# Optimization experiments

Hardware: AMD Instinct MI355X
Metric: run time of the kernel (lower is better)

The kernel has to match this reference:

```python
import jax, jax.numpy as jnp
import numpy as np

B, C, H, E, K, QT = 256, 1024, 64, 64, 2, 20000

def _mlp(x, W1, b1, W2, b2):
    # GKT MLP (eval mode: dropout off; batch-norm omitted, see notes)
    return jax.nn.relu(jax.nn.relu(x @ W1 + b1) @ W2 + b2)

def setup_inputs() -> dict:
    key = jax.random.key(0)
    ks = jax.random.split(key, 30)
    s = 0.05  # weight scale to keep pre-clamp activations in a sane range
    xt = jax.random.uniform(ks[0], (B,), dtype=jnp.float32)
    qt = jax.random.randint(ks[1], (B,), 0, QT)
    ht = jax.random.normal(ks[2], (B, C, H), dtype=jnp.float32)
    # binary question->concept incidence, ~4 KCs per question, col 0 forced on
    oh = (jax.random.uniform(ks[3], (QT, C)) < 4.0 / C).astype(jnp.float32)
    oh = oh.at[:, 0].set(1.0)
    qt_kc_one_hot = jnp.concatenate([oh, jnp.zeros((1, C), jnp.float32)], axis=0)  # zero padding row
    kc_embeddings = jax.random.normal(ks[4], (C, E), dtype=jnp.float32) * 0.1
    graphs = jax.random.uniform(ks[5], (K, C, C), dtype=jnp.float32)  # graph_model output
    neigh_weight = jnp.float32(0.8)
    MI = H + E
    Ws1 = jax.random.normal(ks[6], (MI, H), jnp.float32) * s; bs1 = jnp.zeros((H,), jnp.float32)
    Ws2 = jax.random.normal(ks[7], (H, H), jnp.float32) * s;  bs2 = jnp.zeros((H,), jnp.float32)
    Wn1 = jax.random.normal(ks[8], (K, 2 * MI, H), jnp.float32) * s; bn1 = jnp.zeros((K, H), jnp.float32)
    Wn2 = jax.random.normal(ks[9], (K, H, H), jnp.float32) * s;      bn2 = jnp.zeros((K, H), jnp.float32)
    ea_w = jax.random.uniform(ks[10], (C,), dtype=jnp.float32)
    We = jax.random.normal(ks[11], (H, H), jnp.float32) * s; be = jnp.zeros((H,), jnp.float32)
    Wa = jax.random.normal(ks[12], (H, H), jnp.float32) * s; ba = jnp.zeros((H,), jnp.float32)
    W_ih = jax.random.normal(ks[13], (H, 3 * H), jnp.float32) * s; b_ih = jnp.zeros((3 * H,), jnp.float32)
    W_hh = jax.random.normal(ks[14], (H, 3 * H), jnp.float32) * s; b_hh = jnp.zeros((3 * H,), jnp.float32)
    Wp = jax.random.normal(ks[15], (H, 1), jnp.float32) * s; bp = jnp.zeros((1,), jnp.float32)
    return dict(xt=xt, qt=qt, ht=ht, qt_kc_one_hot=qt_kc_one_hot, kc_embeddings=kc_embeddings,
                graphs=graphs, neigh_weight=neigh_weight, Ws1=Ws1, bs1=bs1, Ws2=Ws2, bs2=bs2,
                Wn1=Wn1, bn1=bn1, Wn2=Wn2, bn2=bn2, ea_w=ea_w, We=We, be=be, Wa=Wa, ba=ba,
                W_ih=W_ih, b_ih=b_ih, W_hh=W_hh, b_hh=b_hh, Wp=Wp, bp=bp)

def reference(xt, qt, ht, qt_kc_one_hot, kc_embeddings, graphs, neigh_weight,
              Ws1, bs1, Ws2, bs2, Wn1, bn1, Wn2, bn2, ea_w, We, be, Wa, ba,
              W_ih, b_ih, W_hh, b_hh, Wp, bp):
    # ---- _aggregate: the fusion loops never write back, so tmp_ht = cat(ht, kc_emb)
    mask = qt_kc_one_hot[qt]                                   # [B, C] gather of binary incidence
    kc = jnp.broadcast_to(kc_embeddings[None], (mask.shape[0], C, E))
    tmp_ht = jnp.concatenate([ht, kc], axis=-1)                # [B, C, H+E]
    # ---- _agg_neighbors
    self_ht = tmp_ht * mask[..., None]
    self_feat = jnp.clip(_mlp(self_ht, Ws1, bs1, Ws2, bs2), -10.0, 10.0)
    neigh_ht = jnp.clip(jnp.concatenate([self_ht, tmp_ht], axis=-1), -5.0, 5.0)  # [B,C,2(H+E)]
    # bug-faithful adj: mean of graphs[k] rows over sample 0's active concepts
    a0 = mask[0]                                               # [C]
    denom = jnp.maximum(a0.sum(), 1.0)
    adj = jnp.clip(jnp.einsum('c,kcd->kd', a0, graphs) / denom, -5.0, 5.0)       # [K, C]
    nb = jax.vmap(lambda W1, b1, W2, b2: _mlp(neigh_ht, W1, b1, W2, b2))(Wn1, bn1, Wn2, bn2)
    nb = jnp.clip(nb, -5.0, 5.0)                               # [K, B, C, H]
    w = jnp.clip(neigh_weight, 0.1, 0.9)
    nf = jnp.clip(adj[0][None, :, None] * nb[0], -5.0, 5.0)
    for k in range(1, K):
        nf = jnp.clip(w * nf + (1.0 - w) * adj[k][None, :, None] * nb[k], -5.0, 5.0)
    m_next = jnp.clip(jnp.where(mask[..., None] > 0.5, self_feat, nf), -50.0, 50.0)
    # ---- erase-add gate
    g = ea_w[None, :, None]
    res = m_next - g * jax.nn.sigmoid(m_next @ We + be) * m_next + g * jnp.tanh(m_next @ Wa + ba)
    # ---- GRUCell over flattened (B*C) rows
    gi = res @ W_ih + b_ih
    gh = ht @ W_hh + b_hh
    ir, iz, in_ = jnp.split(gi, 3, axis=-1)
    hr, hz, hn = jnp.split(gh, 3, axis=-1)
    r = jax.nn.sigmoid(ir + hr)
    z = jax.nn.sigmoid(iz + hz)
    n = jnp.tanh(in_ + r * hn)
    h_next = (1.0 - z) * n + z * ht                            # [B, C, H]
    y = jax.nn.sigmoid(h_next @ Wp + bp)[..., 0]               # [B, C]
    return y
```

## Files before the change

### kernel.cpp

```cpp
#include <hip/hip_runtime.h>

#define DEVINL __device__ __forceinline__

typedef __bf16 bf16x8 __attribute__((ext_vector_type(8)));
typedef float  f32x4  __attribute__((ext_vector_type(4)));
typedef unsigned u32x2 __attribute__((ext_vector_type(2)));

static constexpr size_t kAdjOff  = 0;
static constexpr size_t kBiasOff = 8192;
static constexpr size_t kFragOff = 8192 + 786432;

static constexpr int FB_Wn1h0 = 0,  FB_Wn1h1 = 8,  FB_Wn2_0 = 16, FB_Wn2_1 = 24;
static constexpr int FB_Ws1h  = 32, FB_Ws2   = 40, FB_We    = 48, FB_Wa    = 56;
static constexpr int FB_Wih   = 64, FB_Whh   = 88;

DEVINL unsigned short bf16r(float f) {
  unsigned u = __builtin_bit_cast(unsigned, f);
  unsigned r = ((u >> 16) & 1u) + 0x7FFFu;
  return (unsigned short)((u + r) >> 16);
}
DEVINL float sigmoidf_(float x) { return __builtin_amdgcn_rcpf(1.f + __expf(-x)); }
DEVINL float tanhf_(float x)    { return 1.f - 2.f * __builtin_amdgcn_rcpf(1.f + __expf(2.f * x)); }

DEVINL unsigned pkbf(float a, float b) {
  unsigned d;
  asm("v_cvt_pk_bf16_f32 %0, %1, %2" : "=v"(d) : "v"(a), "v"(b));
  return d;
}

DEVINL f32x4 mfma16(bf16x8 a, bf16x8 b, f32x4 c) {
  return __builtin_amdgcn_mfma_f32_16x16x32_bf16(a, b, c, 0, 0, 0);
}

DEVINL unsigned clip2_(unsigned x) {
  float lo = __builtin_bit_cast(float, x << 16);
  float hi = __builtin_bit_cast(float, x & 0xFFFF0000u);
  lo = fminf(fmaxf(lo, -5.f), 5.f);
  hi = fminf(fmaxf(hi, -5.f), 5.f);
  return (__builtin_bit_cast(unsigned, lo) >> 16) | (__builtin_bit_cast(unsigned, hi) & 0xFFFF0000u);
}
DEVINL bf16x8 clip5(bf16x8 a) {
  uint4 u = __builtin_bit_cast(uint4, a);
  u.x = clip2_(u.x); u.y = clip2_(u.y); u.z = clip2_(u.z); u.w = clip2_(u.w);
  return __builtin_bit_cast(bf16x8, u);
}

DEVINL void ldA2_tr(unsigned addr, bf16x8& a0, bf16x8& a1) {
  u32x2 r0, r1, r2, r3;
  asm volatile(
      "ds_read_b64_tr_b16 %0, %4\n\t"
      "ds_read_b64_tr_b16 %1, %4 offset:512\n\t"
      "ds_read_b64_tr_b16 %2, %4 offset:1024\n\t"
      "ds_read_b64_tr_b16 %3, %4 offset:1536\n\t"
      "s_waitcnt lgkmcnt(0)"
      : "=&v"(r0), "=&v"(r1), "=&v"(r2), "=&v"(r3)
      : "v"(addr)
      : "memory");
  uint4 u0{r0.x, r0.y, r1.x, r1.y};
  uint4 u1{r2.x, r2.y, r3.x, r3.y};
  a0 = __builtin_bit_cast(bf16x8, u0);
  a1 = __builtin_bit_cast(bf16x8, u1);
}

__global__ void prep_adj_kernel(const int* __restrict__ qt, const float* __restrict__ onehot,
                                const float* __restrict__ graphs, float* __restrict__ adjw) {
  __shared__ float a0v[1024];
  __shared__ int   aidx[1024];
  __shared__ int   s_nnz;
  __shared__ float s_den;
  const int tid = threadIdx.x;
  const int k = blockIdx.x >> 2, chunk = blockIdx.x & 3;
  if (tid == 0) { s_nnz = 0; s_den = 0.f; }
  __syncthreads();
  const int q0 = qt[0];
  float lsum = 0.f;
#pragma unroll
  for (int i = 0; i < 4; i++) {
    int c = tid * 4 + i;
    float v = onehot[(size_t)q0 * 1024 + c];
    lsum += v;
    if (v != 0.f) { int p = atomicAdd(&s_nnz, 1); aidx[p] = c; a0v[p] = v; }
  }
#pragma unroll
  for (int off = 32; off >= 1; off >>= 1) lsum += __shfl_xor(lsum, off, 64);
  if ((tid & 63) == 0) atomicAdd(&s_den, lsum);
  __syncthreads();
  const float denom = fmaxf(s_den, 1.f);
  const int nnz = s_nnz;
  const int d = chunk * 256 + tid;
  const float* G = graphs + (size_t)k * 1048576 + d;
  float sum = 0.f;
  for (int j = 0; j < nnz; j++) sum += a0v[j] * G[(size_t)aidx[j] * 1024];
  adjw[k * 1024 + d] = fminf(fmaxf(sum / denom, -5.f), 5.f);
}

__global__ void prep_bias_kernel(const float* __restrict__ kc, const float* __restrict__ Wn1,
                                 const float* __restrict__ bn1, const float* __restrict__ Ws1,
                                 const float* __restrict__ bs1, float* __restrict__ biasTab) {
  int gid = blockIdx.x * 256 + threadIdx.x;
  int j = gid & 63;
  int c = (gid >> 6) & 1023;
  int tab = gid >> 16;
  const float* kcr = kc + (size_t)c * 64;
  float s;
  if (tab < 2) {
    s = bn1[tab * 64 + j];
    const float* W = Wn1 + ((size_t)tab * 256 + 192) * 64 + j;
#pragma unroll 4
    for (int e = 0; e < 64; e++) s += fminf(fmaxf(kcr[e], -5.f), 5.f) * W[(size_t)e * 64];
  } else {
    s = bs1[j];
    const float* W = Ws1 + (size_t)64 * 64 + j;
#pragma unroll 4
    for (int e = 0; e < 64; e++) s += kcr[e] * W[(size_t)e * 64];
  }
  int c16 = c >> 4, rr = c & 3, qq = (c & 15) >> 2, nt = j >> 4;
  int lane = qq * 16 + (j & 15);
  biasTab[(size_t)((((c16 * 3 + tab) * 4 + nt) * 64 + lane)) * 4 + rr] = s;
}

__global__ void prep_wfrag_kernel(const float* __restrict__ Wn1, const float* __restrict__ Wn2,
                                  const float* __restrict__ Ws1, const float* __restrict__ Ws2,
                                  const float* __restrict__ We,  const float* __restrict__ Wa,
                                  const float* __restrict__ Wih, const float* __restrict__ Whh,
                                  uint4* __restrict__ wfrag) {
  const int bid = blockIdx.x, lane = threadIdx.x;
  int mat, ks, nt;
  if (bid < 64) { mat = bid >> 3; ks = (bid >> 2) & 1; nt = bid & 3; }
  else { int f2 = bid - 64; mat = 8 + f2 / 24; int f = f2 % 24; ks = f / 12; nt = f % 12; }
  const float* base = Wn1; int stride = 64;
  switch (mat) {
    case 0: base = Wn1 + (size_t)128 * 64; break;
    case 1: base = Wn1 + (size_t)(256 + 128) * 64; break;
    case 2: base = Wn2; break;
    case 3: base = Wn2 + (size_t)64 * 64; break;
    case 4: base = Ws1; break;
    case 5: base = Ws2; break;
    case 6: base = We; break;
    case 7: base = Wa; break;
    case 8: base = Wih; stride = 192; break;
    case 9: base = Whh; stride = 192; break;
  }
  const int qq = lane >> 4, col = nt * 16 + (lane & 15);
  union { unsigned short u[8]; uint4 v; } tmp;
#pragma unroll
  for (int jj = 0; jj < 8; jj++) {
    int k = ks * 32 + ((jj < 4) ? (qq * 4 + jj) : (16 + qq * 4 + (jj - 4)));
    tmp.u[jj] = bf16r(base[(size_t)k * stride + col]);
  }
  wfrag[(size_t)bid * 64 + lane] = tmp.v;
}

__global__ __launch_bounds__(256, 3) void gkt_main_kernel(
    const int* __restrict__ qt, const float* __restrict__ onehot, const float* __restrict__ ht,
    const float* __restrict__ nw, const float* __restrict__ bn2, const float* __restrict__ be,
    const float* __restrict__ ba, const float* __restrict__ bih, const float* __restrict__ bhh,
    const float* __restrict__ Wp, const float* __restrict__ bp, const float* __restrict__ eaw,
    const float* __restrict__ bs2, const float* __restrict__ adjw, const float* __restrict__ biasTab,
    const bf16x8* __restrict__ wfrag, float* __restrict__ out) {
  __shared__ __align__(128) unsigned short hbuf[4][64][16];
  __shared__ __align__(16) float tokp[4][64];
  __shared__ __align__(16) uint4 gfrag[40 * 64];

  const int tid = threadIdx.x;
  const int wv = tid >> 6, lane = tid & 63;
  const int q = lane >> 4, cl = lane & 15;
  const int t0 = (blockIdx.x * 4 + wv) * 16;
  const int b = t0 >> 10, c0 = t0 & 1023, c16 = c0 >> 4;

  unsigned short* hb = &hbuf[wv][0][0];
  float* tp = &tokp[wv][0];
  const unsigned hbA = (unsigned)(size_t)hb + lane * 8;

  {
    const uint4* wf4 = (const uint4*)wfrag;
#pragma unroll
    for (int i = 0; i < 10; i++) {
      int f = wv * 10 + i;
      gfrag[f * 64 + lane] = wf4[(64 + f) * 64 + lane];
    }
  }

  if (lane < 16) {
    const int c = c0 + lane;
    tp[lane]      = onehot[(size_t)qt[b] * 1024 + c];
    tp[16 + lane] = adjw[c];
    tp[32 + lane] = adjw[1024 + c];
    tp[48 + lane] = eaw[c];
  }
  {
    const float4* ht4 = (const float4*)ht;
#pragma unroll
    for (int i = 0; i < 4; i++) {
      float4 v = ht4[(size_t)t0 * 16 + i * 64 + lane];
      int e = i * 64 + lane;
      int tok = e >> 4, fb = (e & 15) * 4;
      hbuf[wv][fb + 0][tok] = bf16r(v.x);
      hbuf[wv][fb + 1][tok] = bf16r(v.y);
      hbuf[wv][fb + 2][tok] = bf16r(v.z);
      hbuf[wv][fb + 3][tok] = bf16r(v.w);
    }
  }
  __syncthreads();

  const float wmix = fminf(fmaxf(nw[0], 0.1f), 0.9f);

  auto ldB = [&](int frag) -> bf16x8 { return wfrag[frag * 64 + lane]; };
  auto ldG = [&](int fr) -> bf16x8 {
    return (fr < 40) ? *(const bf16x8*)&gfrag[fr * 64 + lane]
                     : wfrag[(64 + fr) * 64 + lane];
  };
  auto ldTP4 = [&](int base) -> f32x4 {
    return *(const f32x4*)(tp + base + q * 4);
  };
  auto packRow = [&](int nt, float v0, float v1, float v2, float v3) {
    unsigned long long d = (unsigned long long)pkbf(v0, v1) |
                           ((unsigned long long)pkbf(v2, v3) << 32);
    *(unsigned long long*)&hbuf[wv][nt * 16 + cl][q * 4] = d;
  };
  const f32x4* bt4 = (const f32x4*)biasTab;

  bf16x8 xr[2];
  ldA2_tr(hbA, xr[0], xr[1]);

  f32x4 nf[4];
  {
    bf16x8 xc[2];
#pragma unroll
    for (int ks = 0; ks < 2; ks++) xc[ks] = clip5(xr[ks]);

#pragma unroll
    for (int k2 = 0; k2 < 2; k2++) {
      f32x4 acc[4];
#pragma unroll
      for (int nt = 0; nt < 4; nt++)
        acc[nt] = bt4[((c16 * 3 + k2) * 4 + nt) * 64 + lane];
#pragma unroll
      for (int ks = 0; ks < 2; ks++)
#pragma unroll
        for (int nt = 0; nt < 4; nt++) {
          bf16x8 bb = ldB((k2 ? FB_Wn1h1 : FB_Wn1h0) + ks * 4 + nt);
          acc[nt] = mfma16(xc[ks], bb, acc[nt]);
        }
#pragma unroll
      for (int nt = 0; nt < 4; nt++)
        packRow(nt, fmaxf(acc[nt][0], 0.f), fmaxf(acc[nt][1], 0.f),
                    fmaxf(acc[nt][2], 0.f), fmaxf(acc[nt][3], 0.f));
      bf16x8 a0, a1;
      ldA2_tr(hbA, a0, a1);
      f32x4 acc2[4];
#pragma unroll
      for (int nt = 0; nt < 4; nt++) {
        float bz = bn2[k2 * 64 + nt * 16 + cl];
        acc2[nt] = {bz, bz, bz, bz};
      }
#pragma unroll
      for (int nt = 0; nt < 4; nt++) {
        acc2[nt] = mfma16(a0, ldB((k2 ? FB_Wn2_1 : FB_Wn2_0) + nt), acc2[nt]);
        acc2[nt] = mfma16(a1, ldB((k2 ? FB_Wn2_1 : FB_Wn2_0) + 4 + nt), acc2[nt]);
      }
      {
        f32x4 adjv = ldTP4((1 + k2) * 16);
#pragma unroll
        for (int nt = 0; nt < 4; nt++)
#pragma unroll
          for (int r = 0; r < 4; r++) {
            float nb = fminf(fmaxf(acc2[nt][r], 0.f), 5.f);
            float v = adjv[r] * nb;
            if (k2 == 0) nf[nt][r] = wmix * fminf(fmaxf(v, -5.f), 5.f);
            else         nf[nt][r] = fminf(fmaxf(nf[nt][r] + (1.f - wmix) * v, -5.f), 5.f);
          }
      }
    }
  }

  bool anySelf = __any((lane < 16) && (tp[lane] > 0.5f));
  if (anySelf) {
    f32x4 acc[4];
#pragma unroll
    for (int nt = 0; nt < 4; nt++)
      acc[nt] = bt4[((c16 * 3 + 2) * 4 + nt) * 64 + lane];
#pragma unroll
    for (int ks = 0; ks < 2; ks++)
#pragma unroll
      for (int nt = 0; nt < 4; nt++) {
        bf16x8 bb = ldB(FB_Ws1h + ks * 4 + nt);
        acc[nt] = mfma16(xr[ks], bb, acc[nt]);
      }
#pragma unroll
    for (int nt = 0; nt < 4; nt++)
      packRow(nt, fmaxf(acc[nt][0], 0.f), fmaxf(acc[nt][1], 0.f),
                  fmaxf(acc[nt][2], 0.f), fmaxf(acc[nt][3], 0.f));
    bf16x8 a0, a1;
    ldA2_tr(hbA, a0, a1);
    f32x4 acc2[4];
#pragma unroll
    for (int nt = 0; nt < 4; nt++) {
      float bz = bs2[nt * 16 + cl];
      acc2[nt] = {bz, bz, bz, bz};
    }
#pragma unroll
    for (int nt = 0; nt < 4; nt++) {
      acc2[nt] = mfma16(a0, ldB(FB_Ws2 + nt), acc2[nt]);
      acc2[nt] = mfma16(a1, ldB(FB_Ws2 + 4 + nt), acc2[nt]);
    }
    {
      f32x4 mk = ldTP4(0);
#pragma unroll
      for (int nt = 0; nt < 4; nt++)
#pragma unroll
        for (int r = 0; r < 4; r++) {
          float sf = fminf(fmaxf(acc2[nt][r], 0.f), 10.f);
          nf[nt][r] = (mk[r] > 0.5f) ? sf : nf[nt][r];
        }
    }
  }

#pragma unroll
  for (int nt = 0; nt < 4; nt++)
    packRow(nt, nf[nt][0], nf[nt][1], nf[nt][2], nf[nt][3]);
  bf16x8 mf[2];
  ldA2_tr(hbA, mf[0], mf[1]);
  {
    f32x4 accE[4];
#pragma unroll
    for (int nt = 0; nt < 4; nt++) {
      float bz = be[nt * 16 + cl];
      accE[nt] = {bz, bz, bz, bz};
    }
#pragma unroll
    for (int ks = 0; ks < 2; ks++)
#pragma unroll
      for (int nt = 0; nt < 4; nt++) {
        bf16x8 bb = ldB(FB_We + ks * 4 + nt);
        accE[nt] = mfma16(mf[ks], bb, accE[nt]);
      }
    {
      f32x4 gv = ldTP4(48);
#pragma unroll
      for (int nt = 0; nt < 4; nt++)
#pragma unroll
        for (int r = 0; r < 4; r++) {
          float m = nf[nt][r];
          nf[nt][r] = m - gv[r] * sigmoidf_(accE[nt][r]) * m;
        }
    }
    f32x4 accA[4];
#pragma unroll
    for (int nt = 0; nt < 4; nt++) {
      float bz = ba[nt * 16 + cl];
      accA[nt] = {bz, bz, bz, bz};
    }
#pragma unroll
    for (int ks = 0; ks < 2; ks++)
#pragma unroll
      for (int nt = 0; nt < 4; nt++) {
        bf16x8 bb = ldB(FB_Wa + ks * 4 + nt);
        accA[nt] = mfma16(mf[ks], bb, accA[nt]);
      }
    {
      f32x4 gv = ldTP4(48);
#pragma unroll
      for (int nt = 0; nt < 4; nt++)
#pragma unroll
        for (int r = 0; r < 4; r++)
          nf[nt][r] += gv[r] * tanhf_(accA[nt][r]);
    }
  }

#pragma unroll
  for (int nt = 0; nt < 4; nt++)
    packRow(nt, nf[nt][0], nf[nt][1], nf[nt][2], nf[nt][3]);
  bf16x8 rf[2];
  ldA2_tr(hbA, rf[0], rf[1]);

  f32x4 gR[4], gZ[4], gN[4], gH[4];
#pragma unroll
  for (int nt = 0; nt < 4; nt++) {
    int col = nt * 16 + cl;
    float brz = bih[col] + bhh[col];
    float bzz = bih[64 + col] + bhh[64 + col];
    float bnn = bih[128 + col];
    float bhn = bhh[128 + col];
    gR[nt] = {brz, brz, brz, brz};
    gZ[nt] = {bzz, bzz, bzz, bzz};
    gN[nt] = {bnn, bnn, bnn, bnn};
    gH[nt] = {bhn, bhn, bhn, bhn};
  }
#pragma unroll
  for (int ks = 0; ks < 2; ks++)
#pragma unroll
    for (int nt = 0; nt < 4; nt++) {
      bf16x8 bi_r = ldG(ks * 12 + nt);
      bf16x8 bh_r = ldG(24 + ks * 12 + nt);
      bf16x8 bi_z = ldG(ks * 12 + 4 + nt);
      bf16x8 bh_z = ldG(24 + ks * 12 + 4 + nt);
      bf16x8 bi_n = ldG(ks * 12 + 8 + nt);
      bf16x8 bh_n = ldG(24 + ks * 12 + 8 + nt);
      gR[nt] = mfma16(rf[ks], bi_r, gR[nt]);
      gR[nt] = mfma16(xr[ks], bh_r, gR[nt]);
      gZ[nt] = mfma16(rf[ks], bi_z, gZ[nt]);
      gZ[nt] = mfma16(xr[ks], bh_z, gZ[nt]);
      gN[nt] = mfma16(rf[ks], bi_n, gN[nt]);
      gH[nt] = mfma16(xr[ks], bh_n, gH[nt]);
    }

  float wp4[4];
#pragma unroll
  for (int nt = 0; nt < 4; nt++) wp4[nt] = Wp[nt * 16 + cl];
  const float bpv = bp[0];

#pragma unroll
  for (int r = 0; r < 4; r++) {
    int tok = q * 4 + r;
    float part = 0.f;
#pragma unroll
    for (int nt = 0; nt < 4; nt++) {
      float rr = sigmoidf_(gR[nt][r]);
      float zz = sigmoidf_(gZ[nt][r]);
      float nval = tanhf_(gN[nt][r] + rr * gH[nt][r]);
      float htv = ht[(size_t)(t0 + tok) * 64 + nt * 16 + cl];
      float hnx = (1.f - zz) * nval + zz * htv;
      part += hnx * wp4[nt];
    }
    part += __shfl_xor(part, 1, 64);
    part += __shfl_xor(part, 2, 64);
    part += __shfl_xor(part, 4, 64);
    part += __shfl_xor(part, 8, 64);
    if (cl == 0) out[t0 + tok] = sigmoidf_(part + bpv);
  }
}

extern "C" void kernel_launch(void* const* d_in, const int* in_sizes, int n_in,
                              void* d_out, int out_size, void* d_ws, size_t ws_size,
                              hipStream_t stream) {
  const int*   qt     = (const int*)d_in[1];
  const float* ht     = (const float*)d_in[2];
  const float* onehot = (const float*)d_in[3];
  const float* kc     = (const float*)d_in[4];
  const float* graphs = (const float*)d_in[5];
  const float* nw     = (const float*)d_in[6];
  const float* Ws1    = (const float*)d_in[7];
  const float* bs1    = (const float*)d_in[8];
  const float* Ws2    = (const float*)d_in[9];
  const float* bs2    = (const float*)d_in[10];
  const float* Wn1    = (const float*)d_in[11];
  const float* bn1    = (const float*)d_in[12];
  const float* Wn2    = (const float*)d_in[13];
  const float* bn2    = (const float*)d_in[14];
  const float* eaw    = (const float*)d_in[15];
  const float* We     = (const float*)d_in[16];
  const float* be     = (const float*)d_in[17];
  const float* Wa     = (const float*)d_in[18];
  const float* ba     = (const float*)d_in[19];
  const float* Wih    = (const float*)d_in[20];
  const float* bih    = (const float*)d_in[21];
  const float* Whh    = (const float*)d_in[22];
  const float* bhh    = (const float*)d_in[23];
  const float* Wp     = (const float*)d_in[24];
  const float* bp     = (const float*)d_in[25];
  float* out = (float*)d_out;

  float* adjw    = (float*)((char*)d_ws + kAdjOff);
  float* biasTab = (float*)((char*)d_ws + kBiasOff);
  uint4* wfragU  = (uint4*)((char*)d_ws + kFragOff);

  prep_adj_kernel<<<8, 256, 0, stream>>>(qt, onehot, graphs, adjw);
  prep_bias_kernel<<<768, 256, 0, stream>>>(kc, Wn1, bn1, Ws1, bs1, biasTab);
  prep_wfrag_kernel<<<112, 64, 0, stream>>>(Wn1, Wn2, Ws1, Ws2, We, Wa, Wih, Whh, wfragU);
  gkt_main_kernel<<<4096, 256, 0, stream>>>(qt, onehot, ht, nw, bn2, be, ba, bih, bhh,
                                            Wp, bp, eaw, bs2, adjw, biasTab,
                                            (const bf16x8*)wfragU, out);
}
```

Before: 270.0 us.

## Compute transposed MFMA chain in registers, two token tiles per wave, no LDS

The main kernel now computes the transposed products (weights as the A operand, activations as B), so each MFMA output feeds the next layer's B operand directly after bf16 packing. This removes the LDS round trips (packRow plus ds_read_b64_tr) and the shared-memory staging of weights and per-token parameters. Each wave now handles 32 tokens as two 16-token streams that share weight fragments, so the grid is halved and launch bounds drop to 2 blocks per SIMD. The bias table layout is changed to match the transposed accumulator layout. The cost is higher register pressure and lower occupancy, and GRU weights are now read from global memory instead of LDS.

```diff
diff --git a/kernel.cpp b/kernel.cpp
--- a/kernel.cpp
+++ b/kernel.cpp
@@ -4,7 +4,6 @@
 
 typedef __bf16 bf16x8 __attribute__((ext_vector_type(8)));
 typedef float  f32x4  __attribute__((ext_vector_type(4)));
-typedef unsigned u32x2 __attribute__((ext_vector_type(2)));
 
 static constexpr size_t kAdjOff  = 0;
 static constexpr size_t kBiasOff = 8192;
@@ -45,21 +44,13 @@
   return __builtin_bit_cast(bf16x8, u);
 }
 
-DEVINL void ldA2_tr(unsigned addr, bf16x8& a0, bf16x8& a1) {
-  u32x2 r0, r1, r2, r3;
-  asm volatile(
-      "ds_read_b64_tr_b16 %0, %4\n\t"
-      "ds_read_b64_tr_b16 %1, %4 offset:512\n\t"
-      "ds_read_b64_tr_b16 %2, %4 offset:1024\n\t"
-      "ds_read_b64_tr_b16 %3, %4 offset:1536\n\t"
-      "s_waitcnt lgkmcnt(0)"
-      : "=&v"(r0), "=&v"(r1), "=&v"(r2), "=&v"(r3)
-      : "v"(addr)
-      : "memory");
-  uint4 u0{r0.x, r0.y, r1.x, r1.y};
-  uint4 u1{r2.x, r2.y, r3.x, r3.y};
-  a0 = __builtin_bit_cast(bf16x8, u0);
-  a1 = __builtin_bit_cast(bf16x8, u1);
+DEVINL bf16x8 d2b(f32x4 lo, f32x4 hi) {
+  uint4 t;
+  t.x = pkbf(lo[0], lo[1]);
+  t.y = pkbf(lo[2], lo[3]);
+  t.z = pkbf(hi[0], hi[1]);
+  t.w = pkbf(hi[2], hi[3]);
+  return __builtin_bit_cast(bf16x8, t);
 }
 
 __global__ void prep_adj_kernel(const int* __restrict__ qt, const float* __restrict__ onehot,
@@ -114,9 +105,8 @@
 #pragma unroll 4
     for (int e = 0; e < 64; e++) s += kcr[e] * W[(size_t)e * 64];
   }
-  int c16 = c >> 4, rr = c & 3, qq = (c & 15) >> 2, nt = j >> 4;
-  int lane = qq * 16 + (j & 15);
-  biasTab[(size_t)((((c16 * 3 + tab) * 4 + nt) * 64 + lane)) * 4 + rr] = s;
+  int c16 = c >> 4, m = j >> 4, qh = (j & 15) >> 2, r = j & 3, tc = c & 15;
+  biasTab[(size_t)((((c16 * 3 + tab) * 4 + m) * 64 + qh * 16 + tc)) * 4 + r] = s;
 }
 
 __global__ void prep_wfrag_kernel(const float* __restrict__ Wn1, const float* __restrict__ Wn2,
@@ -151,284 +141,269 @@
   wfrag[(size_t)bid * 64 + lane] = tmp.v;
 }
 
-__global__ __launch_bounds__(256, 3) void gkt_main_kernel(
+__global__ __launch_bounds__(256, 2) void gkt_main_kernel(
     const int* __restrict__ qt, const float* __restrict__ onehot, const float* __restrict__ ht,
     const float* __restrict__ nw, const float* __restrict__ bn2, const float* __restrict__ be,
     const float* __restrict__ ba, const float* __restrict__ bih, const float* __restrict__ bhh,
     const float* __restrict__ Wp, const float* __restrict__ bp, const float* __restrict__ eaw,
     const float* __restrict__ bs2, const float* __restrict__ adjw, const float* __restrict__ biasTab,
     const bf16x8* __restrict__ wfrag, float* __restrict__ out) {
-  __shared__ __align__(128) unsigned short hbuf[4][64][16];
-  __shared__ __align__(16) float tokp[4][64];
-  __shared__ __align__(16) uint4 gfrag[40 * 64];
-
   const int tid = threadIdx.x;
   const int wv = tid >> 6, lane = tid & 63;
-  const int q = lane >> 4, cl = lane & 15;
-  const int t0 = (blockIdx.x * 4 + wv) * 16;
+  const int q = lane >> 4, tl = lane & 15;
+  const int t0 = (blockIdx.x * 4 + wv) * 32;
   const int b = t0 >> 10, c0 = t0 & 1023, c16 = c0 >> 4;
-
-  unsigned short* hb = &hbuf[wv][0][0];
-  float* tp = &tokp[wv][0];
-  const unsigned hbA = (unsigned)(size_t)hb + lane * 8;
-
+  const int cA = c0 + tl, cB = cA + 16;
+  const size_t gtA = (size_t)t0 + tl, gtB = gtA + 16;
+
+  const int qb = qt[b];
+  const float mkA = onehot[(size_t)qb * 1024 + cA];
+  const float mkB = onehot[(size_t)qb * 1024 + cB];
+  const float adA0 = adjw[cA], adA1 = adjw[1024 + cA];
+  const float adB0 = adjw[cB], adB1 = adjw[1024 + cB];
+  const float gA = eaw[cA], gB = eaw[cB];
+  const float wmix = fminf(fmaxf(nw[0], 0.1f), 0.9f);
+
+  const float4* ht4 = (const float4*)ht;
+  auto loadHtB = [&](size_t gt, int ks) -> bf16x8 {
+    float4 v0 = ht4[gt * 16 + 8 * ks + q];
+    float4 v1 = ht4[gt * 16 + 8 * ks + 4 + q];
+    uint4 t;
+    t.x = pkbf(v0.x, v0.y); t.y = pkbf(v0.z, v0.w);
+    t.z = pkbf(v1.x, v1.y); t.w = pkbf(v1.z, v1.w);
+    return __builtin_bit_cast(bf16x8, t);
+  };
+  bf16x8 xrA[2] = {loadHtB(gtA, 0), loadHtB(gtA, 1)};
+  bf16x8 xrB[2] = {loadHtB(gtB, 0), loadHtB(gtB, 1)};
+
+  auto ldW = [&](int frag) -> bf16x8 { return wfrag[frag * 64 + lane]; };
+  const f32x4* bt4 = (const f32x4*)biasTab;
+
+  f32x4 nfA[4], nfB[4];
+
+  bf16x8 fX[8], fY[8];
+#pragma unroll
+  for (int i = 0; i < 8; i++) fX[i] = ldW(FB_Wn1h0 + i);
+
+#pragma unroll
+  for (int k2 = 0; k2 < 2; k2++) {
+#pragma unroll
+    for (int i = 0; i < 8; i++) fY[i] = ldW((k2 ? FB_Wn2_1 : FB_Wn2_0) + i);
+    bf16x8 xcA[2] = {clip5(xrA[0]), clip5(xrA[1])};
+    bf16x8 xcB[2] = {clip5(xrB[0]), clip5(xrB[1])};
+    f32x4 acA[4], acB[4];
+#pragma unroll
+    for (int m = 0; m < 4; m++) {
+      acA[m] = bt4[(((c16    ) * 3 + k2) * 4 + m) * 64 + lane];
+      acB[m] = bt4[(((c16 + 1) * 3 + k2) * 4 + m) * 64 + lane];
+    }
+#pragma unroll
+    for (int ks = 0; ks < 2; ks++)
+#pragma unroll
+      for (int m = 0; m < 4; m++) {
+        bf16x8 w = fX[ks * 4 + m];
+        acA[m] = mfma16(w, xcA[ks], acA[m]);
+        acB[m] = mfma16(w, xcB[ks], acB[m]);
+      }
+#pragma unroll
+    for (int i = 0; i < 8; i++) fX[i] = ldW((k2 ? FB_Ws1h : FB_Wn1h1) + i);
+    f32x4 r1A[4], r1B[4];
+#pragma unroll
+    for (int m = 0; m < 4; m++)
+#pragma unroll
+      for (int r = 0; r < 4; r++) {
+        r1A[m][r] = fmaxf(acA[m][r], 0.f);
+        r1B[m][r] = fmaxf(acB[m][r], 0.f);
+      }
+    bf16x8 pA0 = d2b(r1A[0], r1A[1]), pA1 = d2b(r1A[2], r1A[3]);
+    bf16x8 pB0 = d2b(r1B[0], r1B[1]), pB1 = d2b(r1B[2], r1B[3]);
+    f32x4 c2A[4], c2B[4];
+#pragma unroll
+    for (int m = 0; m < 4; m++) {
+      f32x4 bz = *(const f32x4*)&bn2[k2 * 64 + m * 16 + q * 4];
+      c2A[m] = bz; c2B[m] = bz;
+    }
+#pragma unroll
+    for (int m = 0; m < 4; m++) {
+      c2A[m] = mfma16(fY[m],     pA0, c2A[m]);
+      c2A[m] = mfma16(fY[4 + m], pA1, c2A[m]);
+      c2B[m] = mfma16(fY[m],     pB0, c2B[m]);
+      c2B[m] = mfma16(fY[4 + m], pB1, c2B[m]);
+    }
+#pragma unroll
+    for (int m = 0; m < 4; m++)
+#pragma unroll
+      for (int r = 0; r < 4; r++) {
+        float nbA = fminf(fmaxf(c2A[m][r], 0.f), 5.f);
+        float nbB = fminf(fmaxf(c2B[m][r], 0.f), 5.f);
+        float vA = (k2 ? adA1 : adA0) * nbA;
+        float vB = (k2 ? adB1 : adB0) * nbB;
+        if (k2 == 0) {
+          nfA[m][r] = wmix * fminf(fmaxf(vA, -5.f), 5.f);
+          nfB[m][r] = wmix * fminf(fmaxf(vB, -5.f), 5.f);
+        } else {
+          nfA[m][r] = fminf(fmaxf(nfA[m][r] + (1.f - wmix) * vA, -5.f), 5.f);
+          nfB[m][r] = fminf(fmaxf(nfB[m][r] + (1.f - wmix) * vB, -5.f), 5.f);
+        }
+      }
+  }
+
+  bool anySelf = __any((mkA > 0.5f) || (mkB > 0.5f));
+  if (anySelf) {
+#pragma unroll
+    for (int i = 0; i < 8; i++) fY[i] = ldW(FB_Ws2 + i);
+    f32x4 acA[4], acB[4];
+#pragma unroll
+    for (int m = 0; m < 4; m++) {
+      acA[m] = bt4[(((c16    ) * 3 + 2) * 4 + m) * 64 + lane];
+      acB[m] = bt4[(((c16 + 1) * 3 + 2) * 4 + m) * 64 + lane];
+    }
+#pragma unroll
+    for (int ks = 0; ks < 2; ks++)
+#pragma unroll
+      for (int m = 0; m < 4; m++) {
+        bf16x8 w = fX[ks * 4 + m];
+        acA[m] = mfma16(w, xrA[ks], acA[m]);
+        acB[m] = mfma16(w, xrB[ks], acB[m]);
+      }
+    f32x4 r1A[4], r1B[4];
+#pragma unroll
+    for (int m = 0; m < 4; m++)
+#pragma unroll
+      for (int r = 0; r < 4; r++) {
+        r1A[m][r] = fmaxf(acA[m][r], 0.f);
+        r1B[m][r] = fmaxf(acB[m][r], 0.f);
+      }
+    bf16x8 pA0 = d2b(r1A[0], r1A[1]), pA1 = d2b(r1A[2], r1A[3]);
+    bf16x8 pB0 = d2b(r1B[0], r1B[1]), pB1 = d2b(r1B[2], r1B[3]);
+    f32x4 c2A[4], c2B[4];
+#pragma unroll
+    for (int m = 0; m < 4; m++) {
+      f32x4 bz = *(const f32x4*)&bs2[m * 16 + q * 4];
+      c2A[m] = bz; c2B[m] = bz;
+    }
+#pragma unroll
+    for (int m = 0; m < 4; m++) {
+      c2A[m] = mfma16(fY[m],     pA0, c2A[m]);
+      c2A[m] = mfma16(fY[4 + m], pA1, c2A[m]);
+      c2B[m] = mfma16(fY[m],     pB0, c2B[m]);
+      c2B[m] = mfma16(fY[4 + m], pB1, c2B[m]);
+    }
+#pragma unroll
+    for (int m = 0; m < 4; m++)
+#pragma unroll
+      for (int r = 0; r < 4; r++) {
+        float sfA = fminf(fmaxf(c2A[m][r], 0.f), 10.f);
+        float sfB = fminf(fmaxf(c2B[m][r], 0.f), 10.f);
+        nfA[m][r] = (mkA > 0.5f) ? sfA : nfA[m][r];
+        nfB[m][r] = (mkB > 0.5f) ? sfB : nfB[m][r];
+      }
+  }
+
+#pragma unroll
+  for (int i = 0; i < 8; i++) fX[i] = ldW(FB_We + i);
+  bf16x8 mA0 = d2b(nfA[0], nfA[1]), mA1 = d2b(nfA[2], nfA[3]);
+  bf16x8 mB0 = d2b(nfB[0], nfB[1]), mB1 = d2b(nfB[2], nfB[3]);
   {
-    const uint4* wf4 = (const uint4*)wfrag;
-#pragma unroll
-    for (int i = 0; i < 10; i++) {
-      int f = wv * 10 + i;
-      gfrag[f * 64 + lane] = wf4[(64 + f) * 64 + lane];
-    }
-  }
-
-  if (lane < 16) {
-    const int c = c0 + lane;
-    tp[lane]      = onehot[(size_t)qt[b] * 1024 + c];
-    tp[16 + lane] = adjw[c];
-    tp[32 + lane] = adjw[1024 + c];
-    tp[48 + lane] = eaw[c];
-  }
-  {
-    const float4* ht4 = (const float4*)ht;
-#pragma unroll
-    for (int i = 0; i < 4; i++) {
-      float4 v = ht4[(size_t)t0 * 16 + i * 64 + lane];
-      int e = i * 64 + lane;
-      int tok = e >> 4, fb = (e & 15) * 4;
-      hbuf[wv][fb + 0][tok] = bf16r(v.x);
-      hbuf[wv][fb + 1][tok] = bf16r(v.y);
-      hbuf[wv][fb + 2][tok] = bf16r(v.z);
-      hbuf[wv][fb + 3][tok] = bf16r(v.w);
-    }
-  }
-  __syncthreads();
-
-  const float wmix = fminf(fmaxf(nw[0], 0.1f), 0.9f);
-
-  auto ldB = [&](int frag) -> bf16x8 { return wfrag[frag * 64 + lane]; };
-  auto ldG = [&](int fr) -> bf16x8 {
-    return (fr < 40) ? *(const bf16x8*)&gfrag[fr * 64 + lane]
-                     : wfrag[(64 + fr) * 64 + lane];
+#pragma unroll
+    for (int i = 0; i < 8; i++) fY[i] = ldW(FB_Wa + i);
+    f32x4 eA[4], eB[4];
+#pragma unroll
+    for (int m = 0; m < 4; m++) {
+      f32x4 bz = *(const f32x4*)&be[m * 16 + q * 4];
+      eA[m] = bz; eB[m] = bz;
+    }
+#pragma unroll
+    for (int m = 0; m < 4; m++) {
+      eA[m] = mfma16(fX[m],     mA0, eA[m]);
+      eA[m] = mfma16(fX[4 + m], mA1, eA[m]);
+      eB[m] = mfma16(fX[m],     mB0, eB[m]);
+      eB[m] = mfma16(fX[4 + m], mB1, eB[m]);
+    }
+#pragma unroll
+    for (int m = 0; m < 4; m++)
+#pragma unroll
+      for (int r = 0; r < 4; r++) {
+        float mAv = nfA[m][r], mBv = nfB[m][r];
+        nfA[m][r] = mAv - gA * sigmoidf_(eA[m][r]) * mAv;
+        nfB[m][r] = mBv - gB * sigmoidf_(eB[m][r]) * mBv;
+      }
+    f32x4 aA[4], aB[4];
+#pragma unroll
+    for (int m = 0; m < 4; m++) {
+      f32x4 bz = *(const f32x4*)&ba[m * 16 + q * 4];
+      aA[m] = bz; aB[m] = bz;
+    }
+#pragma unroll
+    for (int m = 0; m < 4; m++) {
+      aA[m] = mfma16(fY[m],     mA0, aA[m]);
+      aA[m] = mfma16(fY[4 + m], mA1, aA[m]);
+      aB[m] = mfma16(fY[m],     mB0, aB[m]);
+      aB[m] = mfma16(fY[4 + m], mB1, aB[m]);
+    }
+#pragma unroll
+    for (int m = 0; m < 4; m++)
+#pragma unroll
+      for (int r = 0; r < 4; r++) {
+        nfA[m][r] += gA * tanhf_(aA[m][r]);
+        nfB[m][r] += gB * tanhf_(aB[m][r]);
+      }
+  }
+
+  const float bpv = bp[0];
+  auto gruStream = [&](const f32x4* nf, const bf16x8* xr, size_t gt, int tbase) {
+    bf16x8 rf0 = d2b(nf[0], nf[1]), rf1 = d2b(nf[2], nf[3]);
+    f32x4 htv[4], wpv[4], brz[4], bzz[4], bnn[4], bhn[4];
+#pragma unroll
+    for (int m = 0; m < 4; m++) {
+      htv[m] = *(const f32x4*)&ht[gt * 64 + m * 16 + q * 4];
+      wpv[m] = *(const f32x4*)&Wp[m * 16 + q * 4];
+      f32x4 bi0 = *(const f32x4*)&bih[m * 16 + q * 4];
+      f32x4 bh0 = *(const f32x4*)&bhh[m * 16 + q * 4];
+      f32x4 bi1 = *(const f32x4*)&bih[64 + m * 16 + q * 4];
+      f32x4 bh1 = *(const f32x4*)&bhh[64 + m * 16 + q * 4];
+#pragma unroll
+      for (int r = 0; r < 4; r++) {
+        brz[m][r] = bi0[r] + bh0[r];
+        bzz[m][r] = bi1[r] + bh1[r];
+      }
+      bnn[m] = *(const f32x4*)&bih[128 + m * 16 + q * 4];
+      bhn[m] = *(const f32x4*)&bhh[128 + m * 16 + q * 4];
+    }
+    f32x4 gR[4], gZ[4], gN[4], gH[4];
+#pragma unroll
+    for (int m = 0; m < 4; m++) { gR[m] = brz[m]; gZ[m] = bzz[m]; gN[m] = bnn[m]; gH[m] = bhn[m]; }
+#pragma unroll
+    for (int ks = 0; ks < 2; ks++) {
+      bf16x8 rfk = ks ? rf1 : rf0;
+      bf16x8 xrk = xr[ks];
+#pragma unroll
+      for (int m = 0; m < 4; m++) {
+        gR[m] = mfma16(ldW(FB_Wih + ks * 12 + m),     rfk, gR[m]);
+        gR[m] = mfma16(ldW(FB_Whh + ks * 12 + m),     xrk, gR[m]);
+        gZ[m] = mfma16(ldW(FB_Wih + ks * 12 + 4 + m), rfk, gZ[m]);
+        gZ[m] = mfma16(ldW(FB_Whh + ks * 12 + 4 + m), xrk, gZ[m]);
+        gN[m] = mfma16(ldW(FB_Wih + ks * 12 + 8 + m), rfk, gN[m]);
+        gH[m] = mfma16(ldW(FB_Whh + ks * 12 + 8 + m), xrk, gH[m]);
+      }
+    }
+    float part = 0.f;
+#pragma unroll
+    for (int m = 0; m < 4; m++)
+#pragma unroll
+      for (int r = 0; r < 4; r++) {
+        float rr = sigmoidf_(gR[m][r]);
+        float zz = sigmoidf_(gZ[m][r]);
+        float nval = tanhf_(gN[m][r] + rr * gH[m][r]);
+        float hnx = (1.f - zz) * nval + zz * htv[m][r];
+        part += hnx * wpv[m][r];
+      }
+    part += __shfl_xor(part, 16, 64);
+    part += __shfl_xor(part, 32, 64);
+    if (lane < 16) out[t0 + tbase + lane] = sigmoidf_(part + bpv);
   };
-  auto ldTP4 = [&](int base) -> f32x4 {
-    return *(const f32x4*)(tp + base + q * 4);
-  };
-  auto packRow = [&](int nt, float v0, float v1, float v2, float v3) {
-    unsigned long long d = (unsigned long long)pkbf(v0, v1) |
-                           ((unsigned long long)pkbf(v2, v3) << 32);
-    *(unsigned long long*)&hbuf[wv][nt * 16 + cl][q * 4] = d;
-  };
-  const f32x4* bt4 = (const f32x4*)biasTab;
-
-  bf16x8 xr[2];
-  ldA2_tr(hbA, xr[0], xr[1]);
-
-  f32x4 nf[4];
-  {
-    bf16x8 xc[2];
-#pragma unroll
-    for (int ks = 0; ks < 2; ks++) xc[ks] = clip5(xr[ks]);
-
-#pragma unroll
-    for (int k2 = 0; k2 < 2; k2++) {
-      f32x4 acc[4];
-#pragma unroll
-      for (int nt = 0; nt < 4; nt++)
-        acc[nt] = bt4[((c16 * 3 + k2) * 4 + nt) * 64 + lane];
-#pragma unroll
-      for (int ks = 0; ks < 2; ks++)
-#pragma unroll
-        for (int nt = 0; nt < 4; nt++) {
-          bf16x8 bb = ldB((k2 ? FB_Wn1h1 : FB_Wn1h0) + ks * 4 + nt);
-          acc[nt] = mfma16(xc[ks], bb, acc[nt]);
-        }
-#pragma unroll
-      for (int nt = 0; nt < 4; nt++)
-        packRow(nt, fmaxf(acc[nt][0], 0.f), fmaxf(acc[nt][1], 0.f),
-                    fmaxf(acc[nt][2], 0.f), fmaxf(acc[nt][3], 0.f));
-      bf16x8 a0, a1;
-      ldA2_tr(hbA, a0, a1);
-      f32x4 acc2[4];
-#pragma unroll
-      for (int nt = 0; nt < 4; nt++) {
-        float bz = bn2[k2 * 64 + nt * 16 + cl];
-        acc2[nt] = {bz, bz, bz, bz};
-      }
-#pragma unroll
-      for (int nt = 0; nt < 4; nt++) {
-        acc2[nt] = mfma16(a0, ldB((k2 ? FB_Wn2_1 : FB_Wn2_0) + nt), acc2[nt]);
-        acc2[nt] = mfma16(a1, ldB((k2 ? FB_Wn2_1 : FB_Wn2_0) + 4 + nt), acc2[nt]);
-      }
-      {
-        f32x4 adjv = ldTP4((1 + k2) * 16);
-#pragma unroll
-        for (int nt = 0; nt < 4; nt++)
-#pragma unroll
-          for (int r = 0; r < 4; r++) {
-            float nb = fminf(fmaxf(acc2[nt][r], 0.f), 5.f);
-            float v = adjv[r] * nb;
-            if (k2 == 0) nf[nt][r] = wmix * fminf(fmaxf(v, -5.f), 5.f);
-            else         nf[nt][r] = fminf(fmaxf(nf[nt][r] + (1.f - wmix) * v, -5.f), 5.f);
-          }
-      }
-    }
-  }
-
-  bool anySelf = __any((lane < 16) && (tp[lane] > 0.5f));
-  if (anySelf) {
-    f32x4 acc[4];
-#pragma unroll
-    for (int nt = 0; nt < 4; nt++)
-      acc[nt] = bt4[((c16 * 3 + 2) * 4 + nt) * 64 + lane];
-#pragma unroll
-    for (int ks = 0; ks < 2; ks++)
-#pragma unroll
-      for (int nt = 0; nt < 4; nt++) {
-        bf16x8 bb = ldB(FB_Ws1h + ks * 4 + nt);
-        acc[nt] = mfma16(xr[ks], bb, acc[nt]);
-      }
-#pragma unroll
-    for (int nt = 0; nt < 4; nt++)
-      packRow(nt, fmaxf(acc[nt][0], 0.f), fmaxf(acc[nt][1], 0.f),
-                  fmaxf(acc[nt][2], 0.f), fmaxf(acc[nt][3], 0.f));
-    bf16x8 a0, a1;
-    ldA2_tr(hbA, a0, a1);
-    f32x4 acc2[4];
-#pragma unroll
-    for (int nt = 0; nt < 4; nt++) {
-      float bz = bs2[nt * 16 + cl];
-      acc2[nt] = {bz, bz, bz, bz};
-    }
-#pragma unroll
-    for (int nt = 0; nt < 4; nt++) {
-      acc2[nt] = mfma16(a0, ldB(FB_Ws2 + nt), acc2[nt]);
-      acc2[nt] = mfma16(a1, ldB(FB_Ws2 + 4 + nt), acc2[nt]);
-    }
-    {
-      f32x4 mk = ldTP4(0);
-#pragma unroll
-      for (int nt = 0; nt < 4; nt++)
-#pragma unroll
-        for (int r = 0; r < 4; r++) {
-          float sf = fminf(fmaxf(acc2[nt][r], 0.f), 10.f);
-          nf[nt][r] = (mk[r] > 0.5f) ? sf : nf[nt][r];
-        }
-    }
-  }
-
-#pragma unroll
-  for (int nt = 0; nt < 4; nt++)
-    packRow(nt, nf[nt][0], nf[nt][1], nf[nt][2], nf[nt][3]);
-  bf16x8 mf[2];
-  ldA2_tr(hbA, mf[0], mf[1]);
-  {
-    f32x4 accE[4];
-#pragma unroll
-    for (int nt = 0; nt < 4; nt++) {
-      float bz = be[nt * 16 + cl];
-      accE[nt] = {bz, bz, bz, bz};
-    }
-#pragma unroll
-    for (int ks = 0; ks < 2; ks++)
-#pragma unroll
-      for (int nt = 0; nt < 4; nt++) {
-        bf16x8 bb = ldB(FB_We + ks * 4 + nt);
-        accE[nt] = mfma16(mf[ks], bb, accE[nt]);
-      }
-    {
-      f32x4 gv = ldTP4(48);
-#pragma unroll
-      for (int nt = 0; nt < 4; nt++)
-#pragma unroll
-        for (int r = 0; r < 4; r++) {
-          float m = nf[nt][r];
-          nf[nt][r] = m - gv[r] * sigmoidf_(accE[nt][r]) * m;
-        }
-    }
-    f32x4 accA[4];
-#pragma unroll
-    for (int nt = 0; nt < 4; nt++) {
-      float bz = ba[nt * 16 + cl];
-      accA[nt] = {bz, bz, bz, bz};
-    }
-#pragma unroll
-    for (int ks = 0; ks < 2; ks++)
-#pragma unroll
-      for (int nt = 0; nt < 4; nt++) {
-        bf16x8 bb = ldB(FB_Wa + ks * 4 + nt);
-        accA[nt] = mfma16(mf[ks], bb, accA[nt]);
-      }
-    {
-      f32x4 gv = ldTP4(48);
-#pragma unroll
-      for (int nt = 0; nt < 4; nt++)
-#pragma unroll
-        for (int r = 0; r < 4; r++)
-          nf[nt][r] += gv[r] * tanhf_(accA[nt][r]);
-    }
-  }
-
-#pragma unroll
-  for (int nt = 0; nt < 4; nt++)
-    packRow(nt, nf[nt][0], nf[nt][1], nf[nt][2], nf[nt][3]);
-  bf16x8 rf[2];
-  ldA2_tr(hbA, rf[0], rf[1]);
-
-  f32x4 gR[4], gZ[4], gN[4], gH[4];
-#pragma unroll
-  for (int nt = 0; nt < 4; nt++) {
-    int col = nt * 16 + cl;
-    float brz = bih[col] + bhh[col];
-    float bzz = bih[64 + col] + bhh[64 + col];
-    float bnn = bih[128 + col];
-    float bhn = bhh[128 + col];
-    gR[nt] = {brz, brz, brz, brz};
-    gZ[nt] = {bzz, bzz, bzz, bzz};
-    gN[nt] = {bnn, bnn, bnn, bnn};
-    gH[nt] = {bhn, bhn, bhn, bhn};
-  }
-#pragma unroll
-  for (int ks = 0; ks < 2; ks++)
-#pragma unroll
-    for (int nt = 0; nt < 4; nt++) {
-      bf16x8 bi_r = ldG(ks * 12 + nt);
-      bf16x8 bh_r = ldG(24 + ks * 12 + nt);
-      bf16x8 bi_z = ldG(ks * 12 + 4 + nt);
-      bf16x8 bh_z = ldG(24 + ks * 12 + 4 + nt);
-      bf16x8 bi_n = ldG(ks * 12 + 8 + nt);
-      bf16x8 bh_n = ldG(24 + ks * 12 + 8 + nt);
-      gR[nt] = mfma16(rf[ks], bi_r, gR[nt]);
-      gR[nt] = mfma16(xr[ks], bh_r, gR[nt]);
-      gZ[nt] = mfma16(rf[ks], bi_z, gZ[nt]);
-      gZ[nt] = mfma16(xr[ks], bh_z, gZ[nt]);
-      gN[nt] = mfma16(rf[ks], bi_n, gN[nt]);
-      gH[nt] = mfma16(xr[ks], bh_n, gH[nt]);
-    }
-
-  float wp4[4];
-#pragma unroll
-  for (int nt = 0; nt < 4; nt++) wp4[nt] = Wp[nt * 16 + cl];
-  const float bpv = bp[0];
-
-#pragma unroll
-  for (int r = 0; r < 4; r++) {
-    int tok = q * 4 + r;
-    float part = 0.f;
-#pragma unroll
-    for (int nt = 0; nt < 4; nt++) {
-      float rr = sigmoidf_(gR[nt][r]);
-      float zz = sigmoidf_(gZ[nt][r]);
-      float nval = tanhf_(gN[nt][r] + rr * gH[nt][r]);
-      float htv = ht[(size_t)(t0 + tok) * 64 + nt * 16 + cl];
-      float hnx = (1.f - zz) * nval + zz * htv;
-      part += hnx * wp4[nt];
-    }
-    part += __shfl_xor(part, 1, 64);
-    part += __shfl_xor(part, 2, 64);
-    part += __shfl_xor(part, 4, 64);
-    part += __shfl_xor(part, 8, 64);
-    if (cl == 0) out[t0 + tok] = sigmoidf_(part + bpv);
-  }
+  gruStream(nfA, xrA, gtA, 0);
+  gruStream(nfB, xrB, gtB, 16);
 }
 
 extern "C" void kernel_launch(void* const* d_in, const int* in_sizes, int n_in,
@@ -468,7 +443,7 @@
   prep_adj_kernel<<<8, 256, 0, stream>>>(qt, onehot, graphs, adjw);
   prep_bias_kernel<<<768, 256, 0, stream>>>(kc, Wn1, bn1, Ws1, bs1, biasTab);
   prep_wfrag_kernel<<<112, 64, 0, stream>>>(Wn1, Wn2, Ws1, Ws2, We, Wa, Wih, Whh, wfragU);
-  gkt_main_kernel<<<4096, 256, 0, stream>>>(qt, onehot, ht, nw, bn2, be, ba, bih, bhh,
+  gkt_main_kernel<<<2048, 256, 0, stream>>>(qt, onehot, ht, nw, bn2, be, ba, bih, bhh,
                                             Wp, bp, eaw, bs2, adjw, biasTab,
                                             (const bf16x8*)wfragU, out);
 }
```

New measurement: 280.3 us. +3.8%, slower.
